# Kernel optimization log

Hardware: AMD Instinct MI355X
Metric: run time of the kernel (lower is better)

Reference implementation:

```python
import jax, jax.numpy as jnp
import numpy as np

EPS = 1e-12  # torch F.normalize clamp_min eps

def _l2_normalize(x):
    n = jnp.linalg.norm(x, axis=-1, keepdims=True)
    return x / jnp.maximum(n, EPS)

def setup_inputs() -> dict:
    key = jax.random.key(0)
    k1, k2 = jax.random.split(key)
    z_e = jax.random.normal(k1, (32, 256, 32, 32), dtype=jnp.float32)
    weight = jax.random.normal(k2, (1024, 256), dtype=jnp.float32)
    return {"z_e": z_e, "weight": weight}

def reference(z_e, weight):
    B, C, H, W = z_e.shape  # C == embedding_dim
    z = jnp.transpose(z_e, (0, 2, 3, 1))            # [B,H,W,C]
    flat = _l2_normalize(z.reshape(-1, C))          # [N,C]
    w_n = _l2_normalize(weight)                     # [K,C]
    # distances = 2 - 2 * <flat, w_n>; computed without grad in original
    dist = 2.0 - 2.0 * jnp.matmul(flat, w_n.T)      # [N,K]
    idx = jnp.argmin(dist, axis=1)                  # [N]
    z_q = w_n[idx].reshape(B, H, W, C)              # gather codebook rows
    z_q = jnp.transpose(z_q, (0, 3, 1, 2))          # [B,C,H,W]
    indices = idx.reshape(B, H, W)
    return z_q, indices
```

## Files before the change

### kernel.cpp

```cpp
#include <hip/hip_runtime.h>


typedef _Float16 half8 __attribute__((ext_vector_type(8)));
typedef _Float16 half4 __attribute__((ext_vector_type(4)));
typedef float    floatx4 __attribute__((ext_vector_type(4)));

#define C_DIM 256
#define K_CODES 1024
#define HW 1024
#define NPIX 32768
#define NTILES 8
#define USTR 520

#define GLOAD_LDS16(g, l) __builtin_amdgcn_global_load_lds(                    \
    (const __attribute__((address_space(1))) unsigned int*)(g),                \
    (__attribute__((address_space(3))) unsigned int*)(l), 16, 0, 0)

__global__ __launch_bounds__(256) void vq_norm_w(const float* __restrict__ w,
                                                 float* __restrict__ w_n,
                                                 _Float16* __restrict__ wh,
                                                 _Float16* __restrict__ wl) {
    const int row = blockIdx.x;
    const int t   = threadIdx.x;
    float x = w[row * C_DIM + t];
    float s = x * x;
    #pragma unroll
    for (int off = 32; off > 0; off >>= 1) s += __shfl_down(s, off, 64);
    __shared__ float wsum[4];
    if ((t & 63) == 0) wsum[t >> 6] = s;
    __syncthreads();
    float tot = wsum[0] + wsum[1] + wsum[2] + wsum[3];
    float inv = 1.0f / fmaxf(sqrtf(tot), 1e-12f);
    float y = x * inv;
    w_n[row * C_DIM + t] = y;
    float ys = 16.0f * y;
    _Float16 hi = (_Float16)ys;
    wh[row * C_DIM + t] = hi;
    wl[row * C_DIM + t] = (_Float16)(ys - (float)hi);
}

__global__ __launch_bounds__(256, 4) void vq_gemm(
        const float* __restrict__ z,
        const _Float16* __restrict__ wh, const _Float16* __restrict__ wl,
        float* __restrict__ cand_val, int* __restrict__ cand_idx) {
    __shared__ _Float16 Ah[8 * USTR], Al[8 * USTR];
    __shared__ _Float16 Bh[8 * USTR], Bl[8 * USTR];
    __shared__ float red_v[128][2];
    __shared__ int   red_i[128][2];

    const int tid  = threadIdx.x;
    const int lane = tid & 63, wave = tid >> 6;
    const int wm = wave >> 1, wn = wave & 1;
    const int quad = lane >> 4, l15 = lane & 15;
    const int m0 = blockIdx.x * 128, n0 = blockIdx.y * 128;
    const int b  = m0 >> 10, p0 = m0 & 1023;

    const _Float16* bsrc = (wave < 2) ? wh : wl;
    _Float16*       bdst = (wave < 2) ? Bh : Bl;
    const int ub = (wave & 1) * 4;
    const _Float16* gB[4];
    _Float16*       lB[4];
    #pragma unroll
    for (int i = 0; i < 4; i++) {
        gB[i] = bsrc + (size_t)(n0 + (ub + i) * 16 + l15) * C_DIM + quad * 8;
        lB[i] = bdst + (ub + i) * USTR;
    }

    const int ap = (lane & 31) * 4;
    const int as = lane >> 5;
    const int ak = wave * 8 + as * 4;
    const float* zA = z + ((size_t)b * C_DIM + ak) * HW + p0 + ap;

    floatx4 acc[4][4];
    #pragma unroll
    for (int i = 0; i < 4; i++)
        #pragma unroll
        for (int j = 0; j < 4; j++) acc[i][j] = (floatx4){0.f, 0.f, 0.f, 0.f};

    const int afrag = wm * 4, bfrag = wn * 4;

    for (int kt = 0; kt < 8; kt++) {
        __syncthreads();
        #pragma unroll
        for (int i = 0; i < 4; i++)
            GLOAD_LDS16(gB[i] + kt * 32, lB[i]);
        floatx4 za[4];
        #pragma unroll
        for (int r = 0; r < 4; r++)
            za[r] = *(const floatx4*)(zA + (size_t)(kt * 32 + r) * HW);
        #pragma unroll
        for (int i = 0; i < 4; i++) {
            half4 hv, lv;
            #pragma unroll
            for (int r = 0; r < 4; r++) {
                float xv = 4.0f * za[r][i];
                _Float16 h = (_Float16)xv;
                hv[r] = h;
                lv[r] = (_Float16)(xv - (float)h);
            }
            const int p = ap + i;
            const int aidx = (p >> 4) * USTR + wave * 128 + (p & 15) * 8 + as * 4;
            *(half4*)&Ah[aidx] = hv;
            *(half4*)&Al[aidx] = lv;
        }
        __syncthreads();

        half8 ah[4], al[4], bh[4], bl[4];
        #pragma unroll
        for (int i = 0; i < 4; i++) {
            ah[i] = *(const half8*)&Ah[(afrag + i) * USTR + lane * 8];
            al[i] = *(const half8*)&Al[(afrag + i) * USTR + lane * 8];
            bh[i] = *(const half8*)&Bh[(bfrag + i) * USTR + lane * 8];
            bl[i] = *(const half8*)&Bl[(bfrag + i) * USTR + lane * 8];
        }
        #pragma unroll
        for (int mi = 0; mi < 4; mi++)
            #pragma unroll
            for (int ni = 0; ni < 4; ni++) {
                acc[mi][ni] = __builtin_amdgcn_mfma_f32_16x16x32_f16(ah[mi], bh[ni], acc[mi][ni], 0, 0, 0);
                acc[mi][ni] = __builtin_amdgcn_mfma_f32_16x16x32_f16(ah[mi], bl[ni], acc[mi][ni], 0, 0, 0);
                acc[mi][ni] = __builtin_amdgcn_mfma_f32_16x16x32_f16(al[mi], bh[ni], acc[mi][ni], 0, 0, 0);
            }
    }

    #pragma unroll
    for (int mi = 0; mi < 4; mi++) {
        #pragma unroll
        for (int r = 0; r < 4; r++) {
            float bv = -__builtin_inff();
            int   bi = 0x7fffffff;
            #pragma unroll
            for (int ni = 0; ni < 4; ni++) {
                float v = acc[mi][ni][r];
                int  ci = n0 + wn * 64 + ni * 16 + l15;
                if (v > bv || (v == bv && ci < bi)) { bv = v; bi = ci; }
            }
            #pragma unroll
            for (int mk = 8; mk; mk >>= 1) {
                float ov = __shfl_xor(bv, mk, 16);
                int   oi = __shfl_xor(bi, mk, 16);
                if (ov > bv || (ov == bv && oi < bi)) { bv = ov; bi = oi; }
            }
            if (l15 == 0) {
                int row = wm * 64 + mi * 16 + quad * 4 + r;
                red_v[row][wn] = bv;
                red_i[row][wn] = bi;
            }
        }
    }
    __syncthreads();
    if (tid < 128) {
        float bv = red_v[tid][0]; int bi = red_i[tid][0];
        float v2 = red_v[tid][1]; int i2 = red_i[tid][1];
        if (v2 > bv || (v2 == bv && i2 < bi)) { bv = v2; bi = i2; }
        const int pix = m0 + tid;
        cand_val[(size_t)pix * NTILES + blockIdx.y] = bv;
        cand_idx[(size_t)pix * NTILES + blockIdx.y] = bi;
    }
}

__global__ __launch_bounds__(256) void vq_finalize(
        const float* __restrict__ cand_val,
        const int*   __restrict__ cand_idx,
        const float* __restrict__ w_n,
        float* __restrict__ zq,
        float* __restrict__ idx_out) {
    __shared__ float tile[64][257];
    __shared__ int   idx_s[64];
    const int t    = threadIdx.x;
    const int lane = t & 63, wave = t >> 6;
    const int n0   = blockIdx.x * 64;
    const int b    = n0 >> 10, p0 = n0 & 1023;

    if (t < 64) {
        const int n = n0 + t;
        const size_t base = (size_t)n * NTILES;
        float bv = cand_val[base]; int bi = cand_idx[base];
        #pragma unroll
        for (int j = 1; j < NTILES; j++) {
            float v = cand_val[base + j];
            int   c = cand_idx[base + j];
            if (v > bv || (v == bv && c < bi)) { bv = v; bi = c; }
        }
        idx_s[t] = bi;
        idx_out[n] = (float)bi;
    }
    __syncthreads();
    #pragma unroll
    for (int i = 0; i < 16; i++) {
        const int p = wave * 16 + i;
        const int row = idx_s[p];
        floatx4 v = *(const floatx4*)(w_n + (size_t)row * C_DIM + lane * 4);
        *(floatx4*)&tile[p][lane * 4] = v;
    }
    __syncthreads();
    float* zqb = zq + (size_t)b * (C_DIM * HW) + p0;
    #pragma unroll
    for (int it = 0; it < 16; it++) {
        const int c = it * 16 + wave * 4 + (lane >> 4);
        const int p = (lane & 15) * 4;
        floatx4 v = { tile[p][c], tile[p + 1][c], tile[p + 2][c], tile[p + 3][c] };
        *(floatx4*)(zqb + (size_t)c * HW + p) = v;
    }
}

extern "C" void kernel_launch(void* const* d_in, const int* in_sizes, int n_in,
                              void* d_out, int out_size, void* d_ws, size_t ws_size,
                              hipStream_t stream) {
    const float* z = (const float*)d_in[0];
    const float* w = (const float*)d_in[1];
    float* out     = (float*)d_out;

    char* ws = (char*)d_ws;
    float*    w_n  = (float*)(ws);
    _Float16* wh   = (_Float16*)(ws + (1u << 20));
    _Float16* wl   = (_Float16*)(ws + (3u << 19));
    float*    cval = (float*)(ws + (2u << 20));
    int*      cidx = (int*)(ws + (3u << 20));

    vq_norm_w<<<K_CODES, 256, 0, stream>>>(w, w_n, wh, wl);
    vq_gemm<<<dim3(NPIX / 128, NTILES), 256, 0, stream>>>(z, wh, wl, cval, cidx);
    vq_finalize<<<NPIX / 64, 256, 0, stream>>>(cval, cidx, w_n, out, out + 8388608);
}
```

Measured before the change: 155.9 us.

## Fuse finalize into GEMM via packed atomicMax and last-block gather

Removes the separate finalize kernel. Each GEMM block packs its per-pixel best score and code index into a 64-bit key and merges it with atomicMax. A per-row-tile counter picks the last of the NTILES blocks, and that block gathers the codebook rows and writes z_q and the indices. LDS is aliased so the transpose tile reuses the GEMM buffers. This saves one launch and the candidate array round trip, at the cost of atomics, fences, and serialized epilogue work in the last block.

```diff
diff --git a/kernel.cpp b/kernel.cpp
--- a/kernel.cpp
+++ b/kernel.cpp
@@ -19,9 +19,14 @@
 __global__ __launch_bounds__(256) void vq_norm_w(const float* __restrict__ w,
                                                  float* __restrict__ w_n,
                                                  _Float16* __restrict__ wh,
-                                                 _Float16* __restrict__ wl) {
+                                                 _Float16* __restrict__ wl,
+                                                 unsigned long long* __restrict__ pack,
+                                                 unsigned int* __restrict__ cnt) {
     const int row = blockIdx.x;
     const int t   = threadIdx.x;
+    const int gid = row * 256 + t;
+    if (gid < NPIX) pack[gid] = 0ULL;
+    if (gid < 256)  cnt[gid]  = 0u;
     float x = w[row * C_DIM + t];
     float s = x * x;
     #pragma unroll
@@ -42,11 +47,21 @@
 __global__ __launch_bounds__(256, 4) void vq_gemm(
         const float* __restrict__ z,
         const _Float16* __restrict__ wh, const _Float16* __restrict__ wl,
-        float* __restrict__ cand_val, int* __restrict__ cand_idx) {
-    __shared__ _Float16 Ah[8 * USTR], Al[8 * USTR];
-    __shared__ _Float16 Bh[8 * USTR], Bl[8 * USTR];
-    __shared__ float red_v[128][2];
-    __shared__ int   red_i[128][2];
+        const float* __restrict__ w_n,
+        unsigned long long* __restrict__ pack,
+        unsigned int* __restrict__ cnt,
+        float* __restrict__ zq,
+        float* __restrict__ idx_out) {
+    __shared__ __align__(16) char smem[35328];
+    _Float16* Ah = (_Float16*)smem;
+    _Float16* Al = (_Float16*)(smem + 8320);
+    _Float16* Bh = (_Float16*)(smem + 16640);
+    _Float16* Bl = (_Float16*)(smem + 24960);
+    float (*red_v)[2] = (float(*)[2])(smem + 33280);
+    int   (*red_i)[2] = (int  (*)[2])(smem + 34304);
+    float (*tile)[257] = (float(*)[257])smem;
+    __shared__ int idx_s[128];
+    __shared__ int lastflag;
 
     const int tid  = threadIdx.x;
     const int lane = tid & 63, wave = tid >> 6;
@@ -153,54 +168,48 @@
         float bv = red_v[tid][0]; int bi = red_i[tid][0];
         float v2 = red_v[tid][1]; int i2 = red_i[tid][1];
         if (v2 > bv || (v2 == bv && i2 < bi)) { bv = v2; bi = i2; }
-        const int pix = m0 + tid;
-        cand_val[(size_t)pix * NTILES + blockIdx.y] = bv;
-        cand_idx[(size_t)pix * NTILES + blockIdx.y] = bi;
-    }
-}
-
-__global__ __launch_bounds__(256) void vq_finalize(
-        const float* __restrict__ cand_val,
-        const int*   __restrict__ cand_idx,
-        const float* __restrict__ w_n,
-        float* __restrict__ zq,
-        float* __restrict__ idx_out) {
-    __shared__ float tile[64][257];
-    __shared__ int   idx_s[64];
-    const int t    = threadIdx.x;
-    const int lane = t & 63, wave = t >> 6;
-    const int n0   = blockIdx.x * 64;
-    const int b    = n0 >> 10, p0 = n0 & 1023;
-
-    if (t < 64) {
-        const int n = n0 + t;
-        const size_t base = (size_t)n * NTILES;
-        float bv = cand_val[base]; int bi = cand_idx[base];
-        #pragma unroll
-        for (int j = 1; j < NTILES; j++) {
-            float v = cand_val[base + j];
-            int   c = cand_idx[base + j];
-            if (v > bv || (v == bv && c < bi)) { bv = v; bi = c; }
-        }
-        idx_s[t] = bi;
-        idx_out[n] = (float)bi;
-    }
-    __syncthreads();
-    #pragma unroll
-    for (int i = 0; i < 16; i++) {
-        const int p = wave * 16 + i;
-        const int row = idx_s[p];
-        floatx4 v = *(const floatx4*)(w_n + (size_t)row * C_DIM + lane * 4);
-        *(floatx4*)&tile[p][lane * 4] = v;
-    }
-    __syncthreads();
+        unsigned bits = __float_as_uint(bv);
+        unsigned key  = (bits & 0x80000000u) ? ~bits : (bits | 0x80000000u);
+        unsigned long long pkd = ((unsigned long long)key << 32) | (unsigned)(~bi);
+        atomicMax(&pack[m0 + tid], pkd);
+    }
+    __syncthreads();
+    __threadfence();
+    if (tid == 0) {
+        unsigned old = atomicAdd(&cnt[blockIdx.x], 1u);
+        lastflag = (old == NTILES - 1);
+    }
+    __syncthreads();
+    if (!lastflag) return;
+
+    __threadfence();
+    if (tid < 128) {
+        unsigned long long pk = __hip_atomic_load(&pack[m0 + tid],
+                                                  __ATOMIC_ACQUIRE,
+                                                  __HIP_MEMORY_SCOPE_AGENT);
+        int ci = (int)(~(unsigned)pk) & (K_CODES - 1);
+        idx_s[tid] = ci;
+        idx_out[m0 + tid] = (float)ci;
+    }
     float* zqb = zq + (size_t)b * (C_DIM * HW) + p0;
     #pragma unroll
-    for (int it = 0; it < 16; it++) {
-        const int c = it * 16 + wave * 4 + (lane >> 4);
-        const int p = (lane & 15) * 4;
-        floatx4 v = { tile[p][c], tile[p + 1][c], tile[p + 2][c], tile[p + 3][c] };
-        *(floatx4*)(zqb + (size_t)c * HW + p) = v;
+    for (int pass = 0; pass < 4; pass++) {
+        __syncthreads();
+        #pragma unroll
+        for (int i = 0; i < 8; i++) {
+            const int p = wave * 8 + i;
+            const int row = idx_s[pass * 32 + p];
+            floatx4 v = *(const floatx4*)(w_n + (size_t)row * C_DIM + lane * 4);
+            *(floatx4*)&tile[p][lane * 4] = v;
+        }
+        __syncthreads();
+        #pragma unroll
+        for (int it = 0; it < 8; it++) {
+            const int c  = it * 32 + (tid >> 3);
+            const int p4 = (tid & 7) * 4;
+            floatx4 v = { tile[p4][c], tile[p4 + 1][c], tile[p4 + 2][c], tile[p4 + 3][c] };
+            *(floatx4*)(zqb + (size_t)c * HW + pass * 32 + p4) = v;
+        }
     }
 }
 
@@ -215,10 +224,10 @@
     float*    w_n  = (float*)(ws);
     _Float16* wh   = (_Float16*)(ws + (1u << 20));
     _Float16* wl   = (_Float16*)(ws + (3u << 19));
-    float*    cval = (float*)(ws + (2u << 20));
-    int*      cidx = (int*)(ws + (3u << 20));
-
-    vq_norm_w<<<K_CODES, 256, 0, stream>>>(w, w_n, wh, wl);
-    vq_gemm<<<dim3(NPIX / 128, NTILES), 256, 0, stream>>>(z, wh, wl, cval, cidx);
-    vq_finalize<<<NPIX / 64, 256, 0, stream>>>(cval, cidx, w_n, out, out + 8388608);
+    unsigned long long* pack = (unsigned long long*)(ws + (2u << 20));
+    unsigned int*       cnt  = (unsigned int*)(ws + 2359296u);
+
+    vq_norm_w<<<K_CODES, 256, 0, stream>>>(w, w_n, wh, wl, pack, cnt);
+    vq_gemm<<<dim3(NPIX / 128, NTILES), 256, 0, stream>>>(
+        z, wh, wl, w_n, pack, cnt, out, out + 8388608);
 }
```

New measurement: 283.3 us. 81.7% more time.
